# Performance work log

Hardware: AMD Instinct MI355X
Metric: run time of the kernel (lower is better)

The kernel has to match this reference:

```python
import jax, jax.numpy as jnp
import numpy as np

B = 8
NUM_HEADS = 32
HEAD_DIM = 128
EMBED = NUM_HEADS * HEAD_DIM  # 4096
MAX_LEN = 4096
CUR_LEN = 4095  # cache position to write the new token
W_SCALE = 0.02


def setup_inputs() -> dict:
    key = jax.random.key(0)
    ks = jax.random.split(key, 8)
    return {
        "x": jax.random.normal(ks[0], (B, EMBED), jnp.float32),
        "k_cache": jax.random.normal(ks[1], (B, NUM_HEADS, MAX_LEN, HEAD_DIM), jnp.float32),
        "v_cache": jax.random.normal(ks[2], (B, NUM_HEADS, MAX_LEN, HEAD_DIM), jnp.float32),
        "Wq": jax.random.normal(ks[3], (EMBED, EMBED), jnp.float32) * W_SCALE,
        "bq": jnp.zeros((EMBED,), jnp.float32),
        "Wk": jax.random.normal(ks[4], (EMBED, EMBED), jnp.float32) * W_SCALE,
        "bk": jnp.zeros((EMBED,), jnp.float32),
        "Wv": jax.random.normal(ks[5], (EMBED, EMBED), jnp.float32) * W_SCALE,
        "bv": jnp.zeros((EMBED,), jnp.float32),
        "Wo": jax.random.normal(ks[6], (EMBED, EMBED), jnp.float32) * W_SCALE,
        "bo": jnp.zeros((EMBED,), jnp.float32),
        "cur_len": CUR_LEN,
    }


def reference(x, k_cache, v_cache, Wq, bq, Wk, bk, Wv, bv, Wo, bo, cur_len):
    bsz = x.shape[0]
    # QKV projections for the single new token; (B, H, 1, D)
    q = (x @ Wq.T + bq).reshape(bsz, NUM_HEADS, 1, HEAD_DIM)
    k = (x @ Wk.T + bk).reshape(bsz, NUM_HEADS, 1, HEAD_DIM)
    v = (x @ Wv.T + bv).reshape(bsz, NUM_HEADS, 1, HEAD_DIM)
    # KVCache.update: write new k/v at cur_len, then attend over first cur_len+1
    k_cache = k_cache.at[:, :, cur_len:cur_len + 1, :].set(k)
    v_cache = v_cache.at[:, :, cur_len:cur_len + 1, :].set(v)
    full_k = k_cache[:, :, :cur_len + 1, :]  # (B, H, S, D)
    full_v = v_cache[:, :, :cur_len + 1, :]
    scale = 1.0 / jnp.sqrt(jnp.float32(HEAD_DIM))
    scores = jnp.einsum('bhqd,bhkd->bhqk', q, full_k) * scale  # (B, H, 1, S)
    probs = jax.nn.softmax(scores, axis=-1)
    attn = jnp.einsum('bhqk,bhkd->bhqd', probs, full_v)  # (B, H, 1, D)
    attn = attn.reshape(bsz, EMBED)
    return attn @ Wo.T + bo
```

## Files before the change

### kernel.cpp

```cpp
#include <hip/hip_runtime.h>

#define EMBED 4096
#define NHEADS 32
#define HDIM 128
#define MAXLEN 4096
#define BATCH 8
#define NSPLIT 8

template<int RPW>
__device__ __forceinline__ void gemm8_body(const float* __restrict__ X,
                                           const float* __restrict__ W,
                                           const float* __restrict__ bias,
                                           float* __restrict__ out, int n)
{
    const int lane = threadIdx.x & 63;

    float acc[RPW][8];
    #pragma unroll
    for (int j = 0; j < RPW; ++j)
        #pragma unroll
        for (int m = 0; m < 8; ++m) acc[j][m] = 0.f;

    const float* wb = W + (size_t)n * EMBED;

    #pragma unroll 1
    for (int i = 0; i < 16; ++i) {
        int c = i * 256 + lane * 4;
        float4 wv[RPW];
        #pragma unroll
        for (int j = 0; j < RPW; ++j)
            wv[j] = *(const float4*)(wb + (size_t)j * EMBED + c);
        #pragma unroll
        for (int m = 0; m < 8; ++m) {
            float4 xv = *(const float4*)(X + (size_t)m * EMBED + c);
            #pragma unroll
            for (int j = 0; j < RPW; ++j) {
                acc[j][m] += xv.x * wv[j].x + xv.y * wv[j].y
                           + xv.z * wv[j].z + xv.w * wv[j].w;
            }
        }
    }

    #pragma unroll
    for (int j = 0; j < RPW; ++j)
        #pragma unroll
        for (int m = 0; m < 8; ++m) {
            float v = acc[j][m];
            #pragma unroll
            for (int off = 32; off > 0; off >>= 1) v += __shfl_xor(v, off, 64);
            if (lane == 0) out[(size_t)m * EMBED + n + j] = v + bias[n + j];
        }
}

__global__ __launch_bounds__(256)
void qkv_kernel(const float* __restrict__ x,
                const float* __restrict__ Wq, const float* __restrict__ bq,
                const float* __restrict__ Wk, const float* __restrict__ bk,
                const float* __restrict__ Wv, const float* __restrict__ bv,
                float* __restrict__ qkv )
{
    const int wave = threadIdx.x >> 6;
    int ng = blockIdx.x * 16 + wave * 4;
    int proj = ng >> 12;
    int n = ng & 4095;
    const float* W = proj == 0 ? Wq : (proj == 1 ? Wk : Wv);
    const float* b = proj == 0 ? bq : (proj == 1 ? bk : bv);
    float* out = qkv + (size_t)proj * (BATCH * EMBED);
    gemm8_body<4>(x, W, b, out, n);
}

__global__ __launch_bounds__(256)
void out_kernel(const float* __restrict__ attn,
                const float* __restrict__ Wo, const float* __restrict__ bo,
                float* __restrict__ out)
{
    const int wave = threadIdx.x >> 6;
    int n = blockIdx.x * 8 + wave * 2;
    gemm8_body<2>(attn, Wo, bo, out, n);
}

__global__ __launch_bounds__(256)
void attn_partial(const float* __restrict__ qkv,
                  const float* __restrict__ kc, const float* __restrict__ vc,
                  const int* __restrict__ clp,
                  float* __restrict__ part_acc,
                  float* __restrict__ part_ms)
{
    __shared__ float sc[512];
    __shared__ float accw[4 * HDIM];
    __shared__ float redm[4], reds[4];

    const int cl = *clp;
    const int T  = cl + 1;
    const int CH = (T + NSPLIT - 1) / NSPLIT;

    const int bh = blockIdx.x & 255;
    const int sp = blockIdx.x >> 8;
    const int b  = bh >> 5;
    const int h  = bh & 31;
    const int tid = threadIdx.x, w = tid >> 6, lane = tid & 63;
    const int half = lane >> 5, col4 = lane & 31;

    const int tstart = sp * CH;
    const int tend   = min(T, tstart + CH);
    const int len    = tend - tstart;

    const float* q    = qkv + (size_t)b * EMBED + h * HDIM;
    const float* knew = qkv + (size_t)BATCH * EMBED     + (size_t)b * EMBED + h * HDIM;
    const float* vnew = qkv + (size_t)2 * BATCH * EMBED + (size_t)b * EMBED + h * HDIM;
    const float* K = kc + (size_t)bh * MAXLEN * HDIM;
    const float* V = vc + (size_t)bh * MAXLEN * HDIM;

    const float scale = 0.08838834764831845f;
    float4 qv = *(const float4*)(q + col4 * 4);
    qv.x *= scale; qv.y *= scale; qv.z *= scale; qv.w *= scale;

    float lmax = -3.0e38f;
    for (int base = tstart + w * 8; base < tend; base += 32) {
        float4 kv[4];
        #pragma unroll
        for (int u = 0; u < 4; ++u) {
            int t = base + u * 2 + half;
            if (t < tend) {
                const float* p = (t == cl) ? knew : (K + (size_t)t * HDIM);
                kv[u] = *(const float4*)(p + col4 * 4);
            } else {
                kv[u] = make_float4(0.f, 0.f, 0.f, 0.f);
            }
        }
        #pragma unroll
        for (int u = 0; u < 4; ++u) {
            int t = base + u * 2 + half;
            float s = qv.x * kv[u].x + qv.y * kv[u].y + qv.z * kv[u].z + qv.w * kv[u].w;
            #pragma unroll
            for (int off = 16; off > 0; off >>= 1) s += __shfl_xor(s, off, 64);
            if (t < tend) {
                if (col4 == 0) sc[t - tstart] = s;
                lmax = fmaxf(lmax, s);
            }
        }
    }
    lmax = fmaxf(lmax, __shfl_xor(lmax, 32, 64));
    if (lane == 0) redm[w] = lmax;
    __syncthreads();
    float gmax = fmaxf(fmaxf(redm[0], redm[1]), fmaxf(redm[2], redm[3]));

    float lsum = 0.f;
    for (int i = tid; i < len; i += 256) {
        float e = __expf(sc[i] - gmax);
        sc[i] = e;
        lsum += e;
    }
    #pragma unroll
    for (int off = 32; off > 0; off >>= 1) lsum += __shfl_xor(lsum, off, 64);
    if (lane == 0) reds[w] = lsum;
    __syncthreads();
    float csum = reds[0] + reds[1] + reds[2] + reds[3];

    float4 acc = make_float4(0.f, 0.f, 0.f, 0.f);
    for (int base = tstart + w * 8; base < tend; base += 32) {
        float4 vv[4];
        float  pr[4];
        #pragma unroll
        for (int u = 0; u < 4; ++u) {
            int t = base + u * 2 + half;
            if (t < tend) {
                const float* p = (t == cl) ? vnew : (V + (size_t)t * HDIM);
                vv[u] = *(const float4*)(p + col4 * 4);
                pr[u] = sc[t - tstart];
            } else {
                vv[u] = make_float4(0.f, 0.f, 0.f, 0.f);
                pr[u] = 0.f;
            }
        }
        #pragma unroll
        for (int u = 0; u < 4; ++u) {
            acc.x += pr[u] * vv[u].x;
            acc.y += pr[u] * vv[u].y;
            acc.z += pr[u] * vv[u].z;
            acc.w += pr[u] * vv[u].w;
        }
    }
    acc.x += __shfl_xor(acc.x, 32, 64);
    acc.y += __shfl_xor(acc.y, 32, 64);
    acc.z += __shfl_xor(acc.z, 32, 64);
    acc.w += __shfl_xor(acc.w, 32, 64);
    if (half == 0) *(float4*)(accw + w * HDIM + col4 * 4) = acc;
    __syncthreads();

    const size_t pidx = (size_t)bh * NSPLIT + sp;
    if (tid < HDIM) {
        float s = accw[tid] + accw[HDIM + tid] + accw[2 * HDIM + tid] + accw[3 * HDIM + tid];
        part_acc[pidx * HDIM + tid] = s;
    }
    if (tid == 0) {
        part_ms[pidx * 2]     = gmax;
        part_ms[pidx * 2 + 1] = csum;
    }
}

__global__ __launch_bounds__(128)
void combine_kernel(const float* __restrict__ part_acc,
                    const float* __restrict__ part_ms,
                    float* __restrict__ attn)
{
    const int bh = blockIdx.x;
    const int d  = threadIdx.x;

    float m[NSPLIT], s[NSPLIT];
    float gmax = -3.0e38f;
    #pragma unroll
    for (int sp = 0; sp < NSPLIT; ++sp) {
        m[sp] = part_ms[((size_t)bh * NSPLIT + sp) * 2];
        s[sp] = part_ms[((size_t)bh * NSPLIT + sp) * 2 + 1];
        gmax  = fmaxf(gmax, m[sp]);
    }
    float total = 0.f, o = 0.f;
    #pragma unroll
    for (int sp = 0; sp < NSPLIT; ++sp) {
        float wgt = __expf(m[sp] - gmax);
        total += s[sp] * wgt;
        o += part_acc[((size_t)bh * NSPLIT + sp) * HDIM + d] * wgt;
    }
    attn[(size_t)bh * HDIM + d] = o / total;
}

extern "C" void kernel_launch(void* const* d_in, const int* in_sizes, int n_in,
                              void* d_out, int out_size, void* d_ws, size_t ws_size,
                              hipStream_t stream) {
    const float* x  = (const float*)d_in[0];
    const float* kc = (const float*)d_in[1];
    const float* vc = (const float*)d_in[2];
    const float* Wq = (const float*)d_in[3];
    const float* bq = (const float*)d_in[4];
    const float* Wk = (const float*)d_in[5];
    const float* bk = (const float*)d_in[6];
    const float* Wv = (const float*)d_in[7];
    const float* bv = (const float*)d_in[8];
    const float* Wo = (const float*)d_in[9];
    const float* bo = (const float*)d_in[10];
    const int* clp  = (const int*)d_in[11];

    float* out      = (float*)d_out;
    float* qkv      = (float*)d_ws;
    float* attn     = qkv + (size_t)3 * BATCH * EMBED;
    float* part_acc = attn + (size_t)BATCH * EMBED;
    float* part_ms  = part_acc + (size_t)256 * NSPLIT * HDIM;

    hipLaunchKernelGGL(qkv_kernel, dim3(768), dim3(256), 0, stream,
                       x, Wq, bq, Wk, bk, Wv, bv, qkv);
    hipLaunchKernelGGL(attn_partial, dim3(256 * NSPLIT), dim3(256), 0, stream,
                       qkv, kc, vc, clp, part_acc, part_ms);
    hipLaunchKernelGGL(combine_kernel, dim3(256), dim3(128), 0, stream,
                       part_acc, part_ms, attn);
    hipLaunchKernelGGL(out_kernel, dim3(512), dim3(256), 0, stream,
                       attn, Wo, bo, out);
}
```

Before: 268.3 us.

## Fuse attention into single-pass online softmax and double KV split count

Replaces the two-pass score/softmax/PV scheme with a single pass that loads K and V rows together and keeps a running max, sum and accumulator per half-wave group. The per-group partials are merged in shared memory before writing the split result, removing the score scratch buffer and two block barriers. The split count along the sequence goes from 8 to 16 to expose more blocks. The cost is extra exp evaluations per token and more partials for the combine step.

```diff
diff --git a/kernel.cpp b/kernel.cpp
--- a/kernel.cpp
+++ b/kernel.cpp
@@ -5,7 +5,7 @@
 #define HDIM 128
 #define MAXLEN 4096
 #define BATCH 8
-#define NSPLIT 8
+#define NSPLIT 16
 
 template<int RPW>
 __device__ __forceinline__ void gemm8_body(const float* __restrict__ X,
@@ -86,9 +86,8 @@
                   float* __restrict__ part_acc,
                   float* __restrict__ part_ms)
 {
-    __shared__ float sc[512];
-    __shared__ float accw[4 * HDIM];
-    __shared__ float redm[4], reds[4];
+    __shared__ float accs[8][HDIM];
+    __shared__ float mls[8][2];
 
     const int cl = *clp;
     const int T  = cl + 1;
@@ -100,10 +99,10 @@
     const int h  = bh & 31;
     const int tid = threadIdx.x, w = tid >> 6, lane = tid & 63;
     const int half = lane >> 5, col4 = lane & 31;
+    const int g = w * 2 + half;
 
     const int tstart = sp * CH;
     const int tend   = min(T, tstart + CH);
-    const int len    = tend - tstart;
 
     const float* q    = qkv + (size_t)b * EMBED + h * HDIM;
     const float* knew = qkv + (size_t)BATCH * EMBED     + (size_t)b * EMBED + h * HDIM;
@@ -115,87 +114,63 @@
     float4 qv = *(const float4*)(q + col4 * 4);
     qv.x *= scale; qv.y *= scale; qv.z *= scale; qv.w *= scale;
 
-    float lmax = -3.0e38f;
-    for (int base = tstart + w * 8; base < tend; base += 32) {
-        float4 kv[4];
+    float m = -3.0e38f, l = 0.f;
+    float4 acc = make_float4(0.f, 0.f, 0.f, 0.f);
+
+    for (int base = tstart + g; base < tend; base += 32) {
+        float4 kv[4], vv[4];
         #pragma unroll
         for (int u = 0; u < 4; ++u) {
-            int t = base + u * 2 + half;
+            int t = base + u * 8;
             if (t < tend) {
-                const float* p = (t == cl) ? knew : (K + (size_t)t * HDIM);
-                kv[u] = *(const float4*)(p + col4 * 4);
-            } else {
-                kv[u] = make_float4(0.f, 0.f, 0.f, 0.f);
+                const float* kp = (t == cl) ? knew : (K + (size_t)t * HDIM);
+                const float* vp = (t == cl) ? vnew : (V + (size_t)t * HDIM);
+                kv[u] = *(const float4*)(kp + col4 * 4);
+                vv[u] = *(const float4*)(vp + col4 * 4);
             }
         }
         #pragma unroll
         for (int u = 0; u < 4; ++u) {
-            int t = base + u * 2 + half;
-            float s = qv.x * kv[u].x + qv.y * kv[u].y + qv.z * kv[u].z + qv.w * kv[u].w;
-            #pragma unroll
-            for (int off = 16; off > 0; off >>= 1) s += __shfl_xor(s, off, 64);
+            int t = base + u * 8;
             if (t < tend) {
-                if (col4 == 0) sc[t - tstart] = s;
-                lmax = fmaxf(lmax, s);
+                float s = qv.x * kv[u].x + qv.y * kv[u].y
+                        + qv.z * kv[u].z + qv.w * kv[u].w;
+                #pragma unroll
+                for (int off = 16; off > 0; off >>= 1) s += __shfl_xor(s, off, 64);
+                float mn   = fmaxf(m, s);
+                float corr = __expf(m - mn);
+                float p    = __expf(s - mn);
+                l = l * corr + p;
+                acc.x = acc.x * corr + p * vv[u].x;
+                acc.y = acc.y * corr + p * vv[u].y;
+                acc.z = acc.z * corr + p * vv[u].z;
+                acc.w = acc.w * corr + p * vv[u].w;
+                m = mn;
             }
         }
     }
-    lmax = fmaxf(lmax, __shfl_xor(lmax, 32, 64));
-    if (lane == 0) redm[w] = lmax;
-    __syncthreads();
-    float gmax = fmaxf(fmaxf(redm[0], redm[1]), fmaxf(redm[2], redm[3]));
-
-    float lsum = 0.f;
-    for (int i = tid; i < len; i += 256) {
-        float e = __expf(sc[i] - gmax);
-        sc[i] = e;
-        lsum += e;
-    }
-    #pragma unroll
-    for (int off = 32; off > 0; off >>= 1) lsum += __shfl_xor(lsum, off, 64);
-    if (lane == 0) reds[w] = lsum;
-    __syncthreads();
-    float csum = reds[0] + reds[1] + reds[2] + reds[3];
-
-    float4 acc = make_float4(0.f, 0.f, 0.f, 0.f);
-    for (int base = tstart + w * 8; base < tend; base += 32) {
-        float4 vv[4];
-        float  pr[4];
-        #pragma unroll
-        for (int u = 0; u < 4; ++u) {
-            int t = base + u * 2 + half;
-            if (t < tend) {
-                const float* p = (t == cl) ? vnew : (V + (size_t)t * HDIM);
-                vv[u] = *(const float4*)(p + col4 * 4);
-                pr[u] = sc[t - tstart];
-            } else {
-                vv[u] = make_float4(0.f, 0.f, 0.f, 0.f);
-                pr[u] = 0.f;
-            }
-        }
-        #pragma unroll
-        for (int u = 0; u < 4; ++u) {
-            acc.x += pr[u] * vv[u].x;
-            acc.y += pr[u] * vv[u].y;
-            acc.z += pr[u] * vv[u].z;
-            acc.w += pr[u] * vv[u].w;
-        }
-    }
-    acc.x += __shfl_xor(acc.x, 32, 64);
-    acc.y += __shfl_xor(acc.y, 32, 64);
-    acc.z += __shfl_xor(acc.z, 32, 64);
-    acc.w += __shfl_xor(acc.w, 32, 64);
-    if (half == 0) *(float4*)(accw + w * HDIM + col4 * 4) = acc;
+
+    if (col4 == 0) { mls[g][0] = m; mls[g][1] = l; }
+    *(float4*)(&accs[g][col4 * 4]) = acc;
     __syncthreads();
 
     const size_t pidx = (size_t)bh * NSPLIT + sp;
     if (tid < HDIM) {
-        float s = accw[tid] + accw[HDIM + tid] + accw[2 * HDIM + tid] + accw[3 * HDIM + tid];
-        part_acc[pidx * HDIM + tid] = s;
-    }
-    if (tid == 0) {
-        part_ms[pidx * 2]     = gmax;
-        part_ms[pidx * 2 + 1] = csum;
+        float M = mls[0][0];
+        #pragma unroll
+        for (int i = 1; i < 8; ++i) M = fmaxf(M, mls[i][0]);
+        float L = 0.f, o = 0.f;
+        #pragma unroll
+        for (int i = 0; i < 8; ++i) {
+            float wgt = __expf(mls[i][0] - M);
+            L += mls[i][1] * wgt;
+            o += accs[i][tid] * wgt;
+        }
+        part_acc[pidx * HDIM + tid] = o;
+        if (tid == 0) {
+            part_ms[pidx * 2]     = M;
+            part_ms[pidx * 2 + 1] = L;
+        }
     }
 }
 
```

After: 269.3 us. No clear change (+0.4%).
